# Performance work log

Hardware: AMD Instinct MI355X
Metric: run time of the kernel (lower is better)

## Reference

```python
import jax, jax.numpy as jnp
import numpy as np

B, S, P, G, E = 16, 1024, 32, 64, 512
HD = E // 2          # head_dim = 256
SCALE = HD ** -0.5
LAMBDA_INIT = 0.8 - 0.6 * float(np.exp(-0.3 * 0.0))  # depth=0 -> 0.2
EPS = 1e-5


def setup_inputs() -> dict:
    key = jax.random.key(0)
    ks = jax.random.split(key, 12)
    inp = {
        'query': jax.random.normal(ks[0], (B, S, E), jnp.float32),
        'key': jax.random.normal(ks[1], (B, P, G, E), jnp.float32),
        'mask': jax.random.randint(ks[2], (B, S), 0, 2).astype(bool),
        'Wq': jax.random.normal(ks[3], (E, E), jnp.float32) * (E ** -0.5),
        'Wk': jax.random.normal(ks[4], (E, E), jnp.float32) * (E ** -0.5),
        'Wv': jax.random.normal(ks[5], (E, E), jnp.float32) * (E ** -0.5),
        'Wo': jax.random.normal(ks[6], (E, E), jnp.float32) * (E ** -0.5),
        'lq1': jax.random.normal(ks[7], (HD,), jnp.float32) * 0.1,
        'lk1': jax.random.normal(ks[8], (HD,), jnp.float32) * 0.1,
        'lq2': jax.random.normal(ks[9], (HD,), jnp.float32) * 0.1,
        'lk2': jax.random.normal(ks[10], (HD,), jnp.float32) * 0.1,
        'gamma': jnp.ones((E,), jnp.float32),
    }
    return inp


def reference(query, key, mask, Wq, Wk, Wv, Wo, lq1, lk1, lq2, lk2, gamma):
    b, s, e = query.shape
    _, p, g, _ = key.shape
    L = p * g
    key2d = key.reshape(b, L, e)

    Q = (query @ Wq).reshape(b, s, 2, HD).transpose(0, 2, 1, 3) * SCALE  # [B,2,S,hd]
    K = (key2d @ Wk).reshape(b, L, 2, HD).transpose(0, 2, 1, 3)          # [B,2,L,hd]
    V = key2d @ Wv                                                       # [B,L,E]

    scores = jnp.einsum('bhsd,bhld->bhsl', Q, K)                         # [B,2,S,L]
    # masked_fill(~mask, 0.0) with mask broadcast [B,1,S,1]
    scores = jnp.where(mask[:, None, :, None], scores, 0.0)
    attn = jax.nn.softmax(scores, axis=-1)

    lam1 = jnp.exp(jnp.sum(lq1 * lk1))
    lam2 = jnp.exp(jnp.sum(lq2 * lk2))
    lam = lam1 - lam2 + LAMBDA_INIT

    diff = attn[:, 0] - lam * attn[:, 1]                                 # [B,S,L]
    out2d = jnp.einsum('bsl,ble->bse', diff, V)                          # [B,S,E]

    # RMSNorm over last dim with affine gamma
    rms = out2d * jax.lax.rsqrt(jnp.mean(out2d * out2d, axis=-1, keepdims=True) + EPS)
    rms = rms * gamma
    out = (rms * (1.0 - LAMBDA_INIT)) @ Wo                               # [B,S,E]

    return out, diff.reshape(b, s, p, g)
```

## Files before the change

### kernel.cpp

```cpp
#include <hip/hip_runtime.h>
#include <hip/hip_bf16.h>


typedef short short8 __attribute__((ext_vector_type(8)));
typedef __bf16 bf16x8 __attribute__((ext_vector_type(8)));
typedef float f32x4 __attribute__((ext_vector_type(4)));

#define LDS_BYTES 16384
#define OUT0_ELEMS 8388608L

__global__ void probe_kernel(const void* gamma, const void* mask, int* flags)
{
    if (threadIdx.x == 0) {
        unsigned g = *(const unsigned*)gamma;
        flags[0] = (g == 0x3F800000u) ? 1 : 0;
        flags[1] = 0;
    }
    __syncthreads();
    const unsigned* mi = (const unsigned*)mask;
    int bad = 0;
    for (int i = threadIdx.x; i < 4096; i += blockDim.x)
        if (mi[i] > 1u) bad = 1;
    if (bad) atomicOr(&flags[1], 1);
}

__global__ void convert_mask(const void* __restrict__ mask, int* __restrict__ mi,
                             const int* __restrict__ flags)
{
    int i = blockIdx.x * 256 + threadIdx.x;
    if (flags[1]) mi[i] = ((const unsigned char*)mask)[i] ? 1 : 0;
    else          mi[i] = ((const int*)mask)[i] ? 1 : 0;
}

__device__ __forceinline__ float read_elem(const void* p, int i, int isf32)
{
    return isf32 ? ((const float*)p)[i]
                 : __bfloat162float(((const __hip_bfloat16*)p)[i]);
}

__global__ void convert_gamma(const void* __restrict__ gamma, float* __restrict__ g,
                              const int* __restrict__ flags)
{
    int i = blockIdx.x * 256 + threadIdx.x;
    g[i] = read_elem(gamma, i, flags[0]);
}

__global__ void transpose_w(const void* __restrict__ Wq, const void* __restrict__ Wk,
                            const void* __restrict__ Wv, const void* __restrict__ Wo,
                            __hip_bfloat16* __restrict__ dst, const int* __restrict__ flags)
{
    int which = blockIdx.y;
    const void* s = (which == 0) ? Wq : (which == 1) ? Wk : (which == 2) ? Wv : Wo;
    __hip_bfloat16* d = dst + (long)which * 262144;
    int idx = blockIdx.x * 256 + threadIdx.x;
    int k = idx >> 9, n = idx & 511;
    d[n * 512 + k] = __float2bfloat16(read_elem(s, idx, flags[0]));
}

__global__ void lam_kernel(const void* __restrict__ lq1, const void* __restrict__ lk1,
                           const void* __restrict__ lq2, const void* __restrict__ lk2,
                           float* __restrict__ lamp, const int* __restrict__ flags)
{
    int t = threadIdx.x;
    int f = flags[0];
    float s1 = 0.0f, s2 = 0.0f;
#pragma unroll
    for (int j = 0; j < 4; ++j) {
        int idx = t * 4 + j;
        s1 += read_elem(lq1, idx, f) * read_elem(lk1, idx, f);
        s2 += read_elem(lq2, idx, f) * read_elem(lk2, idx, f);
    }
#pragma unroll
    for (int off = 1; off < 64; off <<= 1) {
        s1 += __shfl_xor(s1, off);
        s2 += __shfl_xor(s2, off);
    }
    if (t == 0) *lamp = __expf(s1) - __expf(s2) + 0.2f;
}

__global__ void zero_lst(float* __restrict__ lst)
{
    lst[blockIdx.x * 256 + threadIdx.x] = 0.0f;
}

__device__ __forceinline__ void stage_u(const void* A, long aoff, int lda, int af32,
                                        const __hip_bfloat16* B, int ldb,
                                        int kt, char* smem, int tid)
{
    if (af32) {
#pragma unroll
        for (int j = 0; j < 2; ++j) {
            int chunk = j * 256 + tid;
            const float* g = (const float*)A + aoff + (long)(chunk >> 2) * lda + kt + (chunk & 3) * 8;
            f32x4 x0 = *(const f32x4*)g;
            f32x4 x1 = *(const f32x4*)(g + 4);
            __hip_bfloat16 tmp[8];
#pragma unroll
            for (int t = 0; t < 4; ++t) tmp[t] = __float2bfloat16(x0[t]);
#pragma unroll
            for (int t = 0; t < 4; ++t) tmp[4 + t] = __float2bfloat16(x1[t]);
            *(short8*)(smem + chunk * 16) = *(const short8*)tmp;
        }
    } else {
#pragma unroll
        for (int j = 0; j < 2; ++j) {
            int chunk = j * 256 + tid;
            const __hip_bfloat16* g = (const __hip_bfloat16*)A + aoff
                                    + (long)(chunk >> 2) * lda + kt + (chunk & 3) * 8;
            __builtin_amdgcn_global_load_lds(
                (__attribute__((address_space(1))) void*)g,
                (__attribute__((address_space(3))) void*)(smem + chunk * 16), 16, 0, 0);
        }
    }
#pragma unroll
    for (int j = 0; j < 2; ++j) {
        int chunk = j * 256 + tid;
        const __hip_bfloat16* g = B + (long)(chunk >> 2) * ldb + kt + (chunk & 3) * 8;
        __builtin_amdgcn_global_load_lds(
            (__attribute__((address_space(1))) void*)g,
            (__attribute__((address_space(3))) void*)(smem + 8192 + chunk * 16), 16, 0, 0);
    }
}

__device__ __forceinline__ void mfma_block(char* smem, int tid, f32x4 (&acc)[4][4])
{
    const int lane = tid & 63, wid = tid >> 6;
    const int wm = wid >> 1, wn = wid & 1;
    const int lm = lane & 15, lq = lane >> 4;
    short8 a[4], b[4];
#pragma unroll
    for (int i = 0; i < 4; ++i)
        a[i] = *(const short8*)(smem + (wm * 64 + i * 16 + lm) * 64 + lq * 16);
#pragma unroll
    for (int i = 0; i < 4; ++i)
        b[i] = *(const short8*)(smem + 8192 + (wn * 64 + i * 16 + lm) * 64 + lq * 16);
#pragma unroll
    for (int i = 0; i < 4; ++i)
#pragma unroll
        for (int j = 0; j < 4; ++j)
            acc[i][j] = __builtin_amdgcn_mfma_f32_16x16x32_bf16(
                __builtin_bit_cast(bf16x8, a[i]),
                __builtin_bit_cast(bf16x8, b[j]),
                acc[i][j], 0, 0, 0);
}

__device__ __forceinline__ void zero_acc(f32x4 (&acc)[4][4])
{
#pragma unroll
    for (int i = 0; i < 4; ++i)
#pragma unroll
        for (int j = 0; j < 4; ++j)
#pragma unroll
            for (int r = 0; r < 4; ++r) acc[i][j][r] = 0.0f;
}

__device__ __forceinline__ void tile_gemm_u(const void* A, long aoff, int lda, int af32,
                                            const __hip_bfloat16* B, int ldb, int K,
                                            char* smem, int tid, f32x4 (&acc)[4][4])
{
    zero_acc(acc);
    for (int kt = 0; kt < K; kt += 32) {
        __syncthreads();
        stage_u(A, aoff, lda, af32, B, ldb, kt, smem, tid);
        __syncthreads();
        mfma_block(smem, tid, acc);
    }
}

template <int MODE, int AF>
__launch_bounds__(256, 4)
__global__ void gemm_u(const void* __restrict__ A,
                       const __hip_bfloat16* __restrict__ B,
                       void* __restrict__ C,
                       int K, int lda, int ldb, int ldc,
                       long sA, long sB, long sC, float scale,
                       const int* __restrict__ flags)
{
    __shared__ __align__(16) char smem[LDS_BYTES];
    const int tid = threadIdx.x;
    const int bn = blockIdx.x, bm = blockIdx.y, bz = blockIdx.z;
    const int af32 = AF ? flags[0] : 0;
    const long aoff = (long)bz * sA + (long)bm * 128 * lda;
    const __hip_bfloat16* Bb = B + (long)bz * sB + (long)bn * 128 * ldb;

    f32x4 acc[4][4];
    tile_gemm_u(A, aoff, lda, af32, Bb, ldb, K, smem, tid, acc);

    const int f32o = (MODE == 3) ? flags[0] : 0;
    const int lane = tid & 63, wid = tid >> 6;
    const int wm = wid >> 1, wn = wid & 1;
    const int lm = lane & 15, lq = lane >> 4;
#pragma unroll
    for (int im = 0; im < 4; ++im)
#pragma unroll
        for (int in = 0; in < 4; ++in)
#pragma unroll
            for (int r = 0; r < 4; ++r) {
                int row = bm * 128 + wm * 64 + im * 16 + lq * 4 + r;
                int col = bn * 128 + wn * 64 + in * 16 + lm;
                float v = acc[im][in][r] * scale;
                if (MODE == 0) {
                    ((__hip_bfloat16*)C)[bz * sC + (long)row * ldc + col] = __float2bfloat16(v);
                } else if (MODE == 2) {
                    ((float*)C)[bz * sC + (long)row * ldc + col] = v;
                } else if (MODE == 3) {
                    long idx = bz * sC + (long)row * ldc + col;
                    if (f32o) ((float*)C)[idx] = v;
                    else      ((__hip_bfloat16*)C)[idx] = __float2bfloat16(v);
                } else {
                    int bb = row >> 11, l = row & 2047;
                    ((__hip_bfloat16*)C)[((long)bb * 512 + col) * 2048 + l] = __float2bfloat16(v);
                }
            }
}

__device__ __forceinline__ void score_epilogue(
    f32x4 (&acc)[4][4], char* smem, int tid,
    int nt, int st, int b, int bl, const int* __restrict__ mask,
    float* __restrict__ lstats, __hip_bfloat16* __restrict__ P, int h)
{
    const int lane = tid & 63, wid = tid >> 6;
    const int wm = wid >> 1, wn = wid & 1;
    const int lm = lane & 15, lq = lane >> 4;
    float esum[4][4];
#pragma unroll
    for (int im = 0; im < 4; ++im)
#pragma unroll
        for (int r = 0; r < 4; ++r) {
            int rl = wm * 64 + im * 16 + lq * 4 + r;
            int s  = st * 128 + rl;
            int mv = mask[b * 1024 + s];
            float es = 0.0f;
#pragma unroll
            for (int in = 0; in < 4; ++in) {
                int col = nt * 128 + wn * 64 + in * 16 + lm;
                float sc = mv ? acc[im][in][r] : 0.0f;
                float e  = __expf(sc);
                P[((long)bl * 1024 + s) * 2048 + col] = __float2bfloat16(e);
                float t = e;
                t += __shfl_xor(t, 1);
                t += __shfl_xor(t, 2);
                t += __shfl_xor(t, 4);
                t += __shfl_xor(t, 8);
                es += t;
            }
            esum[im][r] = es;
        }
    __syncthreads();
    float* red = (float*)smem;
    if (lm == 0) {
#pragma unroll
        for (int im = 0; im < 4; ++im)
#pragma unroll
            for (int r = 0; r < 4; ++r)
                red[wn * 128 + wm * 64 + im * 16 + lq * 4 + r] = esum[im][r];
    }
    __syncthreads();
    if (tid < 128)
        atomicAdd(&lstats[((long)(b * 2 + h)) * 1024 + st * 128 + tid],
                  red[tid] + red[128 + tid]);
}

__launch_bounds__(256, 3)
__global__ void score_kernel(const __hip_bfloat16* __restrict__ Q,
                             const __hip_bfloat16* __restrict__ Km,
                             const int* __restrict__ mask,
                             float* __restrict__ lstats,
                             __hip_bfloat16* __restrict__ P0,
                             __hip_bfloat16* __restrict__ P1,
                             int bbase)
{
    __shared__ __align__(16) char smem[LDS_BYTES];
    const int tid = threadIdx.x;
    const int nt = blockIdx.x, st = blockIdx.y, bl = blockIdx.z;
    const int b = bl + bbase;
    const long A0 = ((long)b * 1024 + st * 128) * 512;
    const __hip_bfloat16* B0 = Km + ((long)b * 2048 + nt * 128) * 512;

    f32x4 acc[4][4];
    tile_gemm_u(Q, A0, 512, 0, B0, 512, 256, smem, tid, acc);
    score_epilogue(acc, smem, tid, nt, st, b, bl, mask, lstats, P0, 0);
    tile_gemm_u(Q, A0 + 256, 512, 0, B0 + 256, 512, 256, smem, tid, acc);
    score_epilogue(acc, smem, tid, nt, st, b, bl, mask, lstats, P1, 1);
}

__launch_bounds__(256, 3)
__global__ void dv_fused(const __hip_bfloat16* __restrict__ P0,
                         const __hip_bfloat16* __restrict__ P1,
                         const __hip_bfloat16* __restrict__ Vt,
                         const float* __restrict__ lst,
                         const float* __restrict__ lamp,
                         float* __restrict__ o2d,
                         void* __restrict__ dout,
                         int bbase, const int* __restrict__ flags)
{
    __shared__ __align__(16) char smem[LDS_BYTES];
    const int tid = threadIdx.x;
    const int bn = blockIdx.x, bm = blockIdx.y, bz = blockIdx.z;
    const int b = bz + bbase;
    const float lam = *lamp;

    int srow[2]; float i0[2], i1[2];
#pragma unroll
    for (int j = 0; j < 2; ++j) {
        srow[j] = bm * 128 + j * 64 + (tid >> 2);
        i0[j] = 1.0f / lst[((long)(b * 2)) * 1024 + srow[j]];
        i1[j] = lam  / lst[((long)(b * 2 + 1)) * 1024 + srow[j]];
    }

    const __hip_bfloat16* Bb = Vt + (long)b * (512L * 2048) + (long)bn * 128 * 2048;
    const int f32o = flags[0];
    float* doutF = (float*)dout + OUT0_ELEMS;
    __hip_bfloat16* doutH = (__hip_bfloat16*)dout + OUT0_ELEMS;

    f32x4 acc[4][4];
    zero_acc(acc);

    for (int kt = 0; kt < 2048; kt += 32) {
        __syncthreads();
#pragma unroll
        for (int j = 0; j < 2; ++j) {
            int chunk = j * 256 + tid;
            int kc = kt + (chunk & 3) * 8;
            long off = ((long)bz * 1024 + srow[j]) * 2048 + kc;
            union { short8 v; __hip_bfloat16 h[8]; } u0, u1;
            u0.v = *(const short8*)(P0 + off);
            u1.v = *(const short8*)(P1 + off);
            float d[8];
#pragma unroll
            for (int t = 0; t < 8; ++t)
                d[t] = __bfloat162float(u0.h[t]) * i0[j]
                     - __bfloat162float(u1.h[t]) * i1[j];
            __hip_bfloat16 tmp[8];
#pragma unroll
            for (int t = 0; t < 8; ++t) tmp[t] = __float2bfloat16(d[t]);
            *(short8*)(smem + chunk * 16) = *(const short8*)tmp;
            if (bn == 0) {
                long g = ((long)b * 1024 + srow[j]) * 2048 + kc;
                if (f32o) {
                    f32x4 v0, v1;
#pragma unroll
                    for (int t = 0; t < 4; ++t) { v0[t] = d[t]; v1[t] = d[4 + t]; }
                    *(f32x4*)(doutF + g)     = v0;
                    *(f32x4*)(doutF + g + 4) = v1;
                } else {
                    *(short8*)(doutH + g) = *(const short8*)tmp;
                }
            }
        }
#pragma unroll
        for (int j = 0; j < 2; ++j) {
            int chunk = j * 256 + tid;
            const __hip_bfloat16* g = Bb + (long)(chunk >> 2) * 2048 + kt + (chunk & 3) * 8;
            __builtin_amdgcn_global_load_lds(
                (__attribute__((address_space(1))) void*)g,
                (__attribute__((address_space(3))) void*)(smem + 8192 + chunk * 16), 16, 0, 0);
        }
        __syncthreads();
        mfma_block(smem, tid, acc);
    }

    const int lane = tid & 63, wid = tid >> 6;
    const int wm = wid >> 1, wn = wid & 1;
    const int lm = lane & 15, lq = lane >> 4;
#pragma unroll
    for (int im = 0; im < 4; ++im)
#pragma unroll
        for (int in = 0; in < 4; ++in)
#pragma unroll
            for (int r = 0; r < 4; ++r) {
                int row = bm * 128 + wm * 64 + im * 16 + lq * 4 + r;
                int col = bn * 128 + wn * 64 + in * 16 + lm;
                o2d[((long)b * 1024 + row) * 512 + col] = acc[im][in][r];
            }
}

__global__ void finalize_kernel(__hip_bfloat16* P0,
                                const __hip_bfloat16* __restrict__ P1,
                                const float* __restrict__ lstats,
                                const float* __restrict__ lamp,
                                void* dout, int bbase,
                                const int* __restrict__ flags)
{
    const long row = blockIdx.x;
    const int bl = (int)(row >> 10), s = (int)(row & 1023);
    const int b  = bl + bbase;
    const int tid = threadIdx.x;
    const float lam = *lamp;
    const float i0 = 1.0f / lstats[((long)(b * 2)) * 1024 + s];
    const float i1 = lam  / lstats[((long)(b * 2 + 1)) * 1024 + s];
    const long lbase = row * 2048 + (long)tid * 8;

    union { short8 v; __hip_bfloat16 h[8]; } u0, u1, ub;
    u0.v = *(const short8*)(P0 + lbase);
    u1.v = *(const short8*)(P1 + lbase);
    float d[8];
#pragma unroll
    for (int j = 0; j < 8; ++j)
        d[j] = __bfloat162float(u0.h[j]) * i0 - __bfloat162float(u1.h[j]) * i1;

    const long gidx = ((long)b * 1024 + s) * 2048 + (long)tid * 8;
    if (flags[0]) {
        float* outF = (float*)dout + OUT0_ELEMS;
        f32x4 v0, v1;
#pragma unroll
        for (int j = 0; j < 4; ++j) { v0[j] = d[j]; v1[j] = d[4 + j]; }
        *(f32x4*)(outF + gidx)     = v0;
        *(f32x4*)(outF + gidx + 4) = v1;
    } else {
        __hip_bfloat16* outH = (__hip_bfloat16*)dout + OUT0_ELEMS;
        union { short8 v; __hip_bfloat16 h[8]; } uo;
#pragma unroll
        for (int j = 0; j < 8; ++j) uo.h[j] = __float2bfloat16(d[j]);
        *(short8*)(outH + gidx) = uo.v;
    }
#pragma unroll
    for (int j = 0; j < 8; ++j) ub.h[j] = __float2bfloat16(d[j]);
    *(short8*)(P0 + lbase) = ub.v;
}

__global__ void rmsnorm_kernel(const float* __restrict__ X,
                               const float* __restrict__ gamma,
                               __hip_bfloat16* __restrict__ Y)
{
    long row = blockIdx.x;
    int lane = threadIdx.x;
    const float* x = X + row * 512 + lane * 8;
    f32x4 v0 = *(const f32x4*)x;
    f32x4 v1 = *(const f32x4*)(x + 4);
    float ss = v0[0] * v0[0] + v0[1] * v0[1] + v0[2] * v0[2] + v0[3] * v0[3]
             + v1[0] * v1[0] + v1[1] * v1[1] + v1[2] * v1[2] + v1[3] * v1[3];
#pragma unroll
    for (int off = 1; off < 64; off <<= 1) ss += __shfl_xor(ss, off);
    float rinv = rsqrtf(ss * (1.0f / 512.0f) + 1e-5f) * 0.8f;
#pragma unroll
    for (int j = 0; j < 4; ++j)
        Y[row * 512 + lane * 8 + j] = __float2bfloat16(v0[j] * rinv * gamma[lane * 8 + j]);
#pragma unroll
    for (int j = 0; j < 4; ++j)
        Y[row * 512 + lane * 8 + 4 + j] = __float2bfloat16(v1[j] * rinv * gamma[lane * 8 + 4 + j]);
}

extern "C" void kernel_launch(void* const* d_in, const int* in_sizes, int n_in,
                              void* d_out, int out_size, void* d_ws, size_t ws_size,
                              hipStream_t stream)
{
    const void* query = d_in[0];
    const void* key2d = d_in[1];
    const void* maskp = d_in[2];
    const void* Wq    = d_in[3];
    const void* Wk    = d_in[4];
    const void* Wv    = d_in[5];
    const void* Wo    = d_in[6];
    const void* lq1   = d_in[7];
    const void* lk1   = d_in[8];
    const void* lq2   = d_in[9];
    const void* lk2   = d_in[10];
    const void* gamma = d_in[11];

    char* w = (char*)d_ws;
    __hip_bfloat16* WT    = (__hip_bfloat16*)(w);
    __hip_bfloat16* WqT   = WT;
    __hip_bfloat16* WkT   = WT + 262144;
    __hip_bfloat16* WvT   = WT + 524288;
    __hip_bfloat16* WoT   = WT + 786432;
    float*          lamp  = (float*)(w + 2097152);
    int*            flags = (int*)(w + 2097216);
    float*          gammaF= (float*)(w + 2097280);
    int*            maskI = (int*)(w + 2162688);
    __hip_bfloat16* Qb    = (__hip_bfloat16*)(w + 2228224);
    __hip_bfloat16* Kb    = (__hip_bfloat16*)(w + 19005440);
    __hip_bfloat16* Vt    = (__hip_bfloat16*)(w + 52559872);
    float*          lst   = (float*)(w + 86114304);
    float*          o2d   = (float*)(w + 86245376);
    __hip_bfloat16* rmsb  = (__hip_bfloat16*)(w + 119799808);
    __hip_bfloat16* diffBF= (__hip_bfloat16*)(w + 136577024);
    __hip_bfloat16* P1s   = (__hip_bfloat16*)(w + 103022592);

    const bool hugews = ws_size >= 270794752UL;
    const bool bigws  = ws_size >= 203685888UL;

    probe_kernel<<<1, 256, 0, stream>>>(gamma, maskp, flags);
    convert_mask<<<64, 256, 0, stream>>>(maskp, maskI, flags);
    convert_gamma<<<2, 256, 0, stream>>>(gamma, gammaF, flags);
    transpose_w<<<dim3(1024, 4, 1), 256, 0, stream>>>(Wq, Wk, Wv, Wo, WT, flags);
    lam_kernel<<<1, 64, 0, stream>>>(lq1, lk1, lq2, lk2, lamp, flags);
    zero_lst<<<128, 256, 0, stream>>>(lst);

    gemm_u<0, 1><<<dim3(4, 128, 1), 256, 0, stream>>>(query, WqT, Qb,
        512, 512, 512, 512, 0, 0, 0, 0.0625f, flags);
    gemm_u<0, 1><<<dim3(4, 256, 1), 256, 0, stream>>>(key2d, WkT, Kb,
        512, 512, 512, 512, 0, 0, 0, 1.0f, flags);
    gemm_u<1, 1><<<dim3(4, 256, 1), 256, 0, stream>>>(key2d, WvT, Vt,
        512, 512, 512, 0, 0, 0, 0, 1.0f, flags);

    if (hugews) {
        __hip_bfloat16* P0f = diffBF;
        __hip_bfloat16* P1f = diffBF + 33554432L;
        score_kernel<<<dim3(16, 8, 16), 256, 0, stream>>>(Qb, Kb, maskI, lst,
            P0f, P1f, 0);
        dv_fused<<<dim3(4, 8, 16), 256, 0, stream>>>(P0f, P1f, Vt, lst, lamp,
            o2d, d_out, 0, flags);
    } else if (bigws) {
        __hip_bfloat16* P0h = diffBF;
        __hip_bfloat16* P1h = diffBF + 16777216L;
        for (int h = 0; h < 2; ++h) {
            int bb = h * 8;
            score_kernel<<<dim3(16, 8, 8), 256, 0, stream>>>(Qb, Kb, maskI, lst,
                P0h, P1h, bb);
            dv_fused<<<dim3(4, 8, 8), 256, 0, stream>>>(P0h, P1h, Vt, lst, lamp,
                o2d, d_out, bb, flags);
        }
    } else {
        __hip_bfloat16* scratch = (__hip_bfloat16*)d_out;
        for (int h = 0; h < 2; ++h) {
            int bb = h * 8;
            score_kernel<<<dim3(16, 8, 8), 256, 0, stream>>>(Qb, Kb, maskI, lst,
                scratch, P1s, bb);
            finalize_kernel<<<8192, 256, 0, stream>>>(scratch, P1s, lst, lamp,
                d_out, bb, flags);
            gemm_u<2, 0><<<dim3(4, 8, 8), 256, 0, stream>>>(scratch,
                Vt + (long)bb * 512 * 2048, o2d + (long)bb * 1024 * 512,
                2048, 2048, 2048, 512, 1024L * 2048, 512L * 2048, 1024L * 512, 1.0f, flags);
        }
    }

    rmsnorm_kernel<<<16384, 64, 0, stream>>>(o2d, gammaF, rmsb);

    gemm_u<3, 0><<<dim3(4, 128, 1), 256, 0, stream>>>(rmsb, WoT, d_out,
        512, 512, 512, 512, 0, 0, 1024L * 512, 1.0f, flags);
}
```

Before: 672.1 us.

## Replace dv_fused with wide-N dv kernel computing full E per block

Adds dv_wide, where each block owns 32 query rows and all 512 output columns, so the P0/P1 rows are read and combined into diff only once rather than once per N-tile. This is meant to cut redundant global reads of the large probability buffers and the repeated diff writes. In exchange each block holds fewer rows, has a larger LDS footprint and a 2-block occupancy bound, and only half the threads load A, with no software pipelining of the loads.

```diff
diff --git a/kernel.cpp b/kernel.cpp
--- a/kernel.cpp
+++ b/kernel.cpp
@@ -282,6 +282,111 @@
     score_epilogue(acc, smem, tid, nt, st, b, bl, mask, lstats, P0, 0);
     tile_gemm_u(Q, A0 + 256, 512, 0, B0 + 256, 512, 256, smem, tid, acc);
     score_epilogue(acc, smem, tid, nt, st, b, bl, mask, lstats, P1, 1);
+}
+
+__launch_bounds__(256, 2)
+__global__ void dv_wide(const __hip_bfloat16* __restrict__ P0,
+                        const __hip_bfloat16* __restrict__ P1,
+                        const __hip_bfloat16* __restrict__ Vt,
+                        const float* __restrict__ lst,
+                        const float* __restrict__ lamp,
+                        float* __restrict__ o2d,
+                        void* __restrict__ dout,
+                        const int* __restrict__ flags)
+{
+    __shared__ __align__(16) char smem[36864];
+    const int tid = threadIdx.x;
+    const int bm = blockIdx.x, b = blockIdx.y;
+    const float lam = *lamp;
+
+    const int arow = tid >> 2;
+    const int acol = (tid & 3) * 8;
+    const int srow = bm * 32 + (arow & 31);
+    float i0 = 0.0f, i1 = 0.0f;
+    if (tid < 128) {
+        i0 = 1.0f / lst[((long)(b * 2)) * 1024 + srow];
+        i1 = lam  / lst[((long)(b * 2 + 1)) * 1024 + srow];
+    }
+    const __hip_bfloat16* Bb = Vt + (long)b * (512L * 2048);
+    const int f32o = flags[0];
+    float* doutF = (float*)dout + OUT0_ELEMS;
+    __hip_bfloat16* doutH = (__hip_bfloat16*)dout + OUT0_ELEMS;
+
+    f32x4 acc[2][8];
+#pragma unroll
+    for (int im = 0; im < 2; ++im)
+#pragma unroll
+        for (int in = 0; in < 8; ++in)
+#pragma unroll
+            for (int r = 0; r < 4; ++r) acc[im][in][r] = 0.0f;
+
+    const int lane = tid & 63, wid = tid >> 6;
+    const int lm = lane & 15, lq = lane >> 4;
+
+    for (int kt = 0; kt < 2048; kt += 32) {
+        __syncthreads();
+#pragma unroll
+        for (int j = 0; j < 8; ++j) {
+            int chunk = j * 256 + tid;
+            const __hip_bfloat16* g = Bb + (long)(chunk >> 2) * 2048 + kt + (chunk & 3) * 8;
+            __builtin_amdgcn_global_load_lds(
+                (__attribute__((address_space(1))) void*)g,
+                (__attribute__((address_space(3))) void*)(smem + 4096 + chunk * 16), 16, 0, 0);
+        }
+        float d[8];
+        union { short8 v; __hip_bfloat16 h[8]; } ta;
+        if (tid < 128) {
+            long off = ((long)b * 1024 + srow) * 2048 + kt + acol;
+            union { short8 v; __hip_bfloat16 h[8]; } u0, u1;
+            u0.v = *(const short8*)(P0 + off);
+            u1.v = *(const short8*)(P1 + off);
+#pragma unroll
+            for (int t = 0; t < 8; ++t)
+                d[t] = __bfloat162float(u0.h[t]) * i0 - __bfloat162float(u1.h[t]) * i1;
+#pragma unroll
+            for (int t = 0; t < 8; ++t) ta.h[t] = __float2bfloat16(d[t]);
+            *(short8*)(smem + (arow & 31) * 64 + (tid & 3) * 16) = ta.v;
+        }
+        __syncthreads();
+        if (tid < 128) {
+            long g = ((long)b * 1024 + srow) * 2048 + kt + acol;
+            if (f32o) {
+                f32x4 v0, v1;
+#pragma unroll
+                for (int t = 0; t < 4; ++t) { v0[t] = d[t]; v1[t] = d[4 + t]; }
+                *(f32x4*)(doutF + g)     = v0;
+                *(f32x4*)(doutF + g + 4) = v1;
+            } else {
+                *(short8*)(doutH + g) = ta.v;
+            }
+        }
+        short8 af[2], bf[8];
+#pragma unroll
+        for (int im = 0; im < 2; ++im)
+            af[im] = *(const short8*)(smem + (im * 16 + lm) * 64 + lq * 16);
+#pragma unroll
+        for (int in = 0; in < 8; ++in)
+            bf[in] = *(const short8*)(smem + 4096 + (wid * 128 + in * 16 + lm) * 64 + lq * 16);
+#pragma unroll
+        for (int im = 0; im < 2; ++im)
+#pragma unroll
+            for (int in = 0; in < 8; ++in)
+                acc[im][in] = __builtin_amdgcn_mfma_f32_16x16x32_bf16(
+                    __builtin_bit_cast(bf16x8, af[im]),
+                    __builtin_bit_cast(bf16x8, bf[in]),
+                    acc[im][in], 0, 0, 0);
+    }
+
+#pragma unroll
+    for (int im = 0; im < 2; ++im)
+#pragma unroll
+        for (int in = 0; in < 8; ++in)
+#pragma unroll
+            for (int r = 0; r < 4; ++r) {
+                int row = bm * 32 + im * 16 + lq * 4 + r;
+                int col = wid * 128 + in * 16 + lm;
+                o2d[((long)b * 1024 + row) * 512 + col] = acc[im][in][r];
+            }
 }
 
 __launch_bounds__(256, 3)
@@ -499,8 +604,8 @@
         __hip_bfloat16* P1f = diffBF + 33554432L;
         score_kernel<<<dim3(16, 8, 16), 256, 0, stream>>>(Qb, Kb, maskI, lst,
             P0f, P1f, 0);
-        dv_fused<<<dim3(4, 8, 16), 256, 0, stream>>>(P0f, P1f, Vt, lst, lamp,
-            o2d, d_out, 0, flags);
+        dv_wide<<<dim3(32, 16), 256, 0, stream>>>(P0f, P1f, Vt, lst, lamp,
+            o2d, d_out, flags);
     } else if (bigws) {
         __hip_bfloat16* P0h = diffBF;
         __hip_bfloat16* P1h = diffBF + 16777216L;
```

After: 671.2 us. About the same (-0.1%).
